# Kernel tuning notes

Hardware: AMD Instinct MI355X
Metric: run time of the kernel (lower is better)

The kernel has to match this reference:

```python
import jax, jax.numpy as jnp
import numpy as np

N, E, G, D, L = 100000, 1600000, 64, 128, 4
CLS_HID, NUM_CLASSES = 256, 10
BN_EPS = 1e-5


def setup_inputs() -> dict:
    key = jax.random.key(0)
    ks = jax.random.split(key, 16)
    s = 0.05
    cls_in = D + L * D  # sum(dims) = 640
    return {
        "node_deg": jax.random.randint(ks[0], (N,), 0, D),
        "edge_index": jax.random.randint(ks[1], (2, E), 0, N),
        "batch_vec": jnp.sort(jax.random.randint(ks[2], (N,), 0, G)),
        "eps": jnp.zeros((L,), jnp.float32),  # GINConv train_eps init 0
        "W1": jax.random.normal(ks[3], (L, D, D), jnp.float32) * s,
        "b1": jax.random.normal(ks[4], (L, D), jnp.float32) * s,
        "W2": jax.random.normal(ks[5], (L, D, D), jnp.float32) * s,
        "b2": jax.random.normal(ks[6], (L, D), jnp.float32) * s,
        "bn_g": jnp.ones((L, D), jnp.float32),
        "bn_b": jnp.zeros((L, D), jnp.float32),
        "Wc1": jax.random.normal(ks[7], (cls_in, CLS_HID), jnp.float32) * s,
        "bc1": jax.random.normal(ks[8], (CLS_HID,), jnp.float32) * s,
        "Wc2": jax.random.normal(ks[9], (CLS_HID, NUM_CLASSES), jnp.float32) * s,
        "bc2": jax.random.normal(ks[10], (NUM_CLASSES,), jnp.float32) * s,
    }


def reference(node_deg, edge_index, batch_vec, eps, W1, b1, W2, b2, bn_g, bn_b, Wc1, bc1, Wc2, bc2):
    n = node_deg.shape[0]
    src, dst = edge_index[0], edge_index[1]
    # OneHotEmbedding of node degree -> initial node features [N, D]
    x = jax.nn.one_hot(node_deg, D, dtype=jnp.float32)
    zs = [x]
    for l in range(eps.shape[0]):
        h_in = zs[-1]
        # GINConv: (1+eps)*x + scatter-add of neighbor features
        agg = jax.ops.segment_sum(h_in[src], dst, num_segments=n)
        h = (1.0 + eps[l]) * h_in + agg
        # mlp: lin -> lrelu -> lin
        h = jax.nn.leaky_relu(h @ W1[l] + b1[l])
        h = h @ W2[l] + b2[l]
        # BatchNorm1d over nodes (training-mode batch stats, biased var)
        mean = h.mean(axis=0)
        var = h.var(axis=0)
        h = (h - mean) * jax.lax.rsqrt(var + BN_EPS) * bn_g[l] + bn_b[l]
        zs.append(jax.nn.leaky_relu(h))
    z = jnp.concatenate(zs, axis=1)  # [N, 640]
    pooled = jax.ops.segment_sum(z, batch_vec, num_segments=G)  # global_add_pool
    pooled = jax.nn.leaky_relu(pooled)
    # classifier head: Linear -> LeakyReLU -> Linear (drop_out=0)
    h = jax.nn.leaky_relu(pooled @ Wc1 + bc1)
    return h @ Wc2 + bc2
```

## Files before the change

kernel.cpp:

```cpp
#include <hip/hip_runtime.h>
#include <hip/hip_bf16.h>


#define N_NODES   100000
#define N_EDGES   1600000
#define N_GRAPHS  64
#define DIM       128
#define N_LAYERS  4
#define CLS_IN    640
#define CLS_HID   256
#define N_CLASSES 10
#define LRELU_SLOPE 0.01f
#define BN_EPS_F    1e-5f

#define NBUCK    782
#define BUCK_CAP 4096

typedef __attribute__((ext_vector_type(8))) short bf16x8;
typedef __attribute__((ext_vector_type(4))) float f32x4;

__device__ __forceinline__ float lrelu(float x) { return x > 0.f ? x : LRELU_SLOPE * x; }

__device__ __forceinline__ uint pack2(float x, float y) {
    uint a = __float_as_uint(x), b = __float_as_uint(y);
    a = (a + 0x7FFFu + ((a >> 16) & 1u)) >> 16;
    b = (b + 0x7FFFu + ((b >> 16) & 1u)) >> 16;
    return a | (b << 16);
}
__device__ __forceinline__ float2 unpack2(uint v) {
    return make_float2(__uint_as_float(v << 16), __uint_as_float(v & 0xFFFF0000u));
}

__global__ void k_convert_w(const float* __restrict__ W1, const float* __restrict__ W2,
                            ushort* __restrict__ W1t, ushort* __restrict__ W2t) {
    int gid = blockIdx.x * blockDim.x + threadIdx.x;
    if (gid >= 8 * DIM * DIM) return;
    int mat = gid >> 14, idx = gid & 16383;
    int k = idx >> 7, n = idx & 127;
    const float* src = (mat < 4) ? (W1 + mat * DIM * DIM) : (W2 + (mat - 4) * DIM * DIM);
    ushort* dst = (mat < 4) ? (W1t + mat * DIM * DIM) : (W2t + (mat - 4) * DIM * DIM);
    uint a = __float_as_uint(src[k * DIM + n]);
    dst[n * DIM + k] = (ushort)((a + 0x7FFFu + ((a >> 16) & 1u)) >> 16);
}

__global__ void k_build_x(const int* __restrict__ deg, uint* __restrict__ x) {
    int gid = blockIdx.x * blockDim.x + threadIdx.x;
    if (gid >= N_NODES * 64) return;
    int i = gid >> 6, c = gid & 63;
    int d = deg[i];
    uint v = 0;
    if ((d >> 1) == c) v = 0x3F80u << (16 * (d & 1));
    x[gid] = v;
}

__global__ void k_deg_pool(const int* __restrict__ deg, const int* __restrict__ batch,
                           float* __restrict__ pooled) {
    int i = blockIdx.x * blockDim.x + threadIdx.x;
    if (i < N_NODES) atomicAdd(&pooled[batch[i] * CLS_IN + deg[i]], 1.0f);
}

__global__ void __launch_bounds__(1024) k_partition(const int* __restrict__ src,
                                                    const int* __restrict__ dst,
                                                    uint* __restrict__ cursor,
                                                    uint* __restrict__ ebuf) {
    __shared__ uint hist[NBUCK];
    __shared__ uint basev[NBUCK];
    int t = threadIdx.x;
    for (int b = t; b < NBUCK; b += 1024) hist[b] = 0;
    __syncthreads();
    int e0 = blockIdx.x * 16384;
    uint msrc[16], mdst[16], mrank[16];
#pragma unroll
    for (int i = 0; i < 16; ++i) {
        int e = e0 + i * 1024 + t;
        if (e < N_EDGES) {
            msrc[i] = (uint)src[e];
            mdst[i] = (uint)dst[e];
            mrank[i] = atomicAdd(&hist[mdst[i] >> 7], 1u);
        } else mdst[i] = 0xFFFFFFFFu;
    }
    __syncthreads();
    for (int b = t; b < NBUCK; b += 1024) {
        uint c = hist[b];
        basev[b] = c ? (uint)(b * BUCK_CAP) + atomicAdd(&cursor[b], c) : 0u;
    }
    __syncthreads();
#pragma unroll
    for (int i = 0; i < 16; ++i) {
        if (mdst[i] != 0xFFFFFFFFu) {
            uint b = mdst[i] >> 7;
            ebuf[basev[b] + mrank[i]] = ((mdst[i] & 127u) << 17) | msrc[i];
        }
    }
}

__global__ void __launch_bounds__(512) k_agg(const uint* __restrict__ h,
                                             const uint* __restrict__ ebuf,
                                             const uint* __restrict__ cursor,
                                             uint* __restrict__ out,
                                             const float* __restrict__ epsv, int layer) {
    __shared__ uint sortedL[BUCK_CAP];
    __shared__ uint hist[128];
    __shared__ uint startv[129];
    const int t = threadIdx.x, lane = t & 63, wave = t >> 6;
    const int b = blockIdx.x;
    int cnt = (int)cursor[b]; if (cnt > BUCK_CAP) cnt = BUCK_CAP;
    if (t < 128) hist[t] = 0;
    __syncthreads();
    uint ent[8], rank[8];
    const uint* ep = ebuf + b * BUCK_CAP;
#pragma unroll
    for (int k = 0; k < 8; ++k) {
        int i = t + k * 512;
        if (i < cnt) { ent[k] = ep[i]; rank[k] = atomicAdd(&hist[ent[k] >> 17], 1u); }
    }
    __syncthreads();
    if (t < 128) startv[t + 1] = hist[t];
    if (t == 0) startv[0] = 0;
    __syncthreads();
    for (int off = 1; off < 128; off <<= 1) {
        uint add = (t < 128 && t >= off) ? startv[t + 1 - off] : 0u;
        __syncthreads();
        if (t < 128 && t >= off) startv[t + 1] += add;
        __syncthreads();
    }
#pragma unroll
    for (int k = 0; k < 8; ++k) {
        int i = t + k * 512;
        if (i < cnt) sortedL[startv[ent[k] >> 17] + rank[k]] = ent[k];
    }
    __syncthreads();
    const float s = 1.0f + epsv[layer];
    const int node0 = b * 128;
    for (int ri = 0; ri < 16; ++ri) {
        int r = wave * 16 + ri;
        int g = node0 + r;
        if (g >= N_NODES) break;
        int beg = (int)startv[r], end = (int)startv[r + 1];
        float2 own = unpack2(h[g * 64 + lane]);
        float ax = s * own.x, ay = s * own.y;
        int j = beg;
        for (; j + 4 <= end; j += 4) {
            uint u0 = sortedL[j]     & 0x1FFFFu;
            uint u1 = sortedL[j + 1] & 0x1FFFFu;
            uint u2 = sortedL[j + 2] & 0x1FFFFu;
            uint u3 = sortedL[j + 3] & 0x1FFFFu;
            uint h0 = h[u0 * 64 + lane], h1 = h[u1 * 64 + lane];
            uint h2 = h[u2 * 64 + lane], h3 = h[u3 * 64 + lane];
            float2 f0 = unpack2(h0), f1 = unpack2(h1), f2 = unpack2(h2), f3 = unpack2(h3);
            ax += (f0.x + f1.x) + (f2.x + f3.x);
            ay += (f0.y + f1.y) + (f2.y + f3.y);
        }
        for (; j < end; ++j) {
            uint u = sortedL[j] & 0x1FFFFu;
            float2 f = unpack2(h[u * 64 + lane]);
            ax += f.x; ay += f.y;
        }
        out[g * 64 + lane] = pack2(ax, ay);
    }
}

#define GEMM_LDS_BYTES 69632
__global__ void __launch_bounds__(256) k_gemm(const ushort* __restrict__ A,
                                              const ushort* __restrict__ Wt,
                                              const float* __restrict__ bias,
                                              ushort* __restrict__ C,
                                              float* __restrict__ stats,
                                              int do_lrelu) {
    __shared__ char pool[GEMM_LDS_BYTES];
    ushort* As = (ushort*)pool;
    ushort* Ws = (ushort*)(pool + 34816);
    float*  Cs = (float*)pool;
    const int t = threadIdx.x;
    const int row0 = blockIdx.x * 128;
    {
        int r = t >> 1, hh = t & 1;
        uint4* l = (uint4*)(As + r * 136 + hh * 64);
        if (row0 + r < N_NODES) {
            const uint4* g = (const uint4*)(A + (size_t)(row0 + r) * DIM + hh * 64);
#pragma unroll
            for (int k = 0; k < 8; ++k) l[k] = g[k];
        } else {
            uint4 z = make_uint4(0, 0, 0, 0);
#pragma unroll
            for (int k = 0; k < 8; ++k) l[k] = z;
        }
        const uint4* gw = (const uint4*)(Wt + r * DIM + hh * 64);
        uint4* lw = (uint4*)(Ws + r * 136 + hh * 64);
#pragma unroll
        for (int k = 0; k < 8; ++k) lw[k] = gw[k];
    }
    __syncthreads();
    const int lane = t & 63, wave = t >> 6;
    const int q = lane >> 4, m = lane & 15;
    const int R = (wave >> 1) * 64, Cb = (wave & 1) * 64;
    f32x4 acc[4][4] = {};
#pragma unroll
    for (int ks = 0; ks < 4; ++ks) {
        bf16x8 a[4], b[4];
#pragma unroll
        for (int i = 0; i < 4; ++i)
            a[i] = *(const bf16x8*)(As + (R + i * 16 + m) * 136 + ks * 32 + q * 8);
#pragma unroll
        for (int j = 0; j < 4; ++j)
            b[j] = *(const bf16x8*)(Ws + (Cb + j * 16 + m) * 136 + ks * 32 + q * 8);
#pragma unroll
        for (int i = 0; i < 4; ++i)
#pragma unroll
            for (int j = 0; j < 4; ++j)
                acc[i][j] = __builtin_amdgcn_mfma_f32_16x16x32_bf16(a[i], b[j], acc[i][j], 0, 0, 0);
    }
    __syncthreads();
    float biasr[4];
#pragma unroll
    for (int j = 0; j < 4; ++j) biasr[j] = bias[Cb + j * 16 + m];
#pragma unroll
    for (int i = 0; i < 4; ++i)
#pragma unroll
        for (int j = 0; j < 4; ++j)
#pragma unroll
            for (int r = 0; r < 4; ++r)
                Cs[(R + i * 16 + q * 4 + r) * 132 + Cb + j * 16 + m] = acc[i][j][r] + biasr[j];
    __syncthreads();
    if (stats != nullptr && t < DIM) {
        int rows = N_NODES - row0; if (rows > 128) rows = 128;
        float s1 = 0.f, s2 = 0.f;
        for (int r = 0; r < rows; ++r) { float v = Cs[r * 132 + t]; s1 += v; s2 += v * v; }
        atomicAdd(&stats[t], s1);
        atomicAdd(&stats[DIM + t], s2);
    }
    {
        int r = t >> 1, hh = t & 1;
        if (row0 + r < N_NODES) {
            uint4* outp = (uint4*)(C + (size_t)(row0 + r) * DIM + hh * 64);
#pragma unroll
            for (int k = 0; k < 8; ++k) {
                float4 v0 = *(const float4*)(Cs + r * 132 + hh * 64 + k * 8);
                float4 v1 = *(const float4*)(Cs + r * 132 + hh * 64 + k * 8 + 4);
                if (do_lrelu) {
                    v0.x = lrelu(v0.x); v0.y = lrelu(v0.y); v0.z = lrelu(v0.z); v0.w = lrelu(v0.w);
                    v1.x = lrelu(v1.x); v1.y = lrelu(v1.y); v1.z = lrelu(v1.z); v1.w = lrelu(v1.w);
                }
                uint4 o;
                o.x = pack2(v0.x, v0.y); o.y = pack2(v0.z, v0.w);
                o.z = pack2(v1.x, v1.y); o.w = pack2(v1.z, v1.w);
                outp[k] = o;
            }
        }
    }
}

__global__ void k_bn_final(float* __restrict__ stats, const float* __restrict__ bn_g,
                           const float* __restrict__ bn_b, int layer) {
    int f = threadIdx.x;
    float mean = stats[f] * (1.0f / N_NODES);
    float var  = stats[DIM + f] * (1.0f / N_NODES) - mean * mean;
    float inv  = rsqrtf(var + BN_EPS_F);
    float sc = bn_g[layer * DIM + f] * inv;
    float sh = bn_b[layer * DIM + f] - mean * sc;
    stats[f] = sc;
    stats[DIM + f] = sh;
}

#define PROWS 128
__global__ void __launch_bounds__(256) k_bnpool(const uint* __restrict__ src,
                                                uint* __restrict__ dst,
                                                const float* __restrict__ stats,
                                                const int* __restrict__ batch,
                                                float* __restrict__ pooled, int colOff) {
    int c = threadIdx.x & 63;
    int chunk = threadIdx.x >> 6;
    int r0 = blockIdx.x * PROWS + chunk * (PROWS / 4);
    float sc0 = stats[2 * c], sc1 = stats[2 * c + 1];
    float sh0 = stats[DIM + 2 * c], sh1 = stats[DIM + 2 * c + 1];
    int curg = -1;
    float a0 = 0.f, a1 = 0.f;
    for (int i = 0; i < PROWS / 4; ++i) {
        int r = r0 + i;
        if (r >= N_NODES) break;
        float2 v = unpack2(src[r * 64 + c]);
        float x0 = lrelu(v.x * sc0 + sh0);
        float x1 = lrelu(v.y * sc1 + sh1);
        dst[r * 64 + c] = pack2(x0, x1);
        int g = batch[r];
        if (g != curg) {
            if (curg >= 0) {
                atomicAdd(&pooled[curg * CLS_IN + colOff + 2 * c], a0);
                atomicAdd(&pooled[curg * CLS_IN + colOff + 2 * c + 1], a1);
            }
            curg = g; a0 = 0.f; a1 = 0.f;
        }
        a0 += x0; a1 += x1;
    }
    if (curg >= 0) {
        atomicAdd(&pooled[curg * CLS_IN + colOff + 2 * c], a0);
        atomicAdd(&pooled[curg * CLS_IN + colOff + 2 * c + 1], a1);
    }
}

__global__ void __launch_bounds__(256) k_classifier(const float* __restrict__ pooled,
                                                    const float* __restrict__ Wc1,
                                                    const float* __restrict__ bc1,
                                                    const float* __restrict__ Wc2,
                                                    const float* __restrict__ bc2,
                                                    float* __restrict__ out) {
    __shared__ float p[CLS_IN];
    __shared__ float hh[CLS_HID];
    int g = blockIdx.x, t = threadIdx.x;
    for (int j = t; j < CLS_IN; j += 256) p[j] = lrelu(pooled[g * CLS_IN + j]);
    __syncthreads();
    float acc = bc1[t];
    for (int k = 0; k < CLS_IN; ++k) acc += p[k] * Wc1[k * CLS_HID + t];
    hh[t] = lrelu(acc);
    __syncthreads();
    if (t < N_CLASSES) {
        float a2 = bc2[t];
        for (int k = 0; k < CLS_HID; ++k) a2 += hh[k] * Wc2[k * N_CLASSES + t];
        out[g * N_CLASSES + t] = a2;
    }
}

extern "C" void kernel_launch(void* const* d_in, const int* in_sizes, int n_in,
                              void* d_out, int out_size, void* d_ws, size_t ws_size,
                              hipStream_t stream) {
    const int*   deg   = (const int*)d_in[0];
    const int*   edges = (const int*)d_in[1];
    const int*   srcv  = edges;
    const int*   dstv  = edges + N_EDGES;
    const int*   batch = (const int*)d_in[2];
    const float* epsv  = (const float*)d_in[3];
    const float* W1    = (const float*)d_in[4];
    const float* b1    = (const float*)d_in[5];
    const float* W2    = (const float*)d_in[6];
    const float* b2    = (const float*)d_in[7];
    const float* bn_g  = (const float*)d_in[8];
    const float* bn_b  = (const float*)d_in[9];
    const float* Wc1   = (const float*)d_in[10];
    const float* bc1   = (const float*)d_in[11];
    const float* Wc2   = (const float*)d_in[12];
    const float* bc2   = (const float*)d_in[13];

    char* ws = (char*)d_ws;
    const size_t BUFB = (size_t)N_NODES * DIM * 2;
    size_t off = 0;
    ushort* buf0   = (ushort*)(ws + off); off += BUFB;
    ushort* buf1   = (ushort*)(ws + off); off += BUFB;
    ushort* W1t    = (ushort*)(ws + off); off += 4 * DIM * DIM * 2;
    ushort* W2t    = (ushort*)(ws + off); off += 4 * DIM * DIM * 2;
    float*  pooled = (float*)(ws + off);  off += N_GRAPHS * CLS_IN * 4;
    float*  statsA = (float*)(ws + off);  off += 4 * 2 * DIM * 4;
    uint*   cursor = (uint*)(ws + off);   off += (NBUCK + 8) * 4;
    uint*   ebuf   = (uint*)(ws + off);   off += (size_t)NBUCK * BUCK_CAP * 4;

    hipMemsetAsync(pooled, 0, N_GRAPHS * CLS_IN * 4, stream);
    hipMemsetAsync(statsA, 0, 4 * 2 * DIM * 4, stream);
    hipMemsetAsync(cursor, 0, NBUCK * 4, stream);

    k_convert_w<<<(8 * DIM * DIM + 255) / 256, 256, 0, stream>>>(W1, W2, W1t, W2t);
    k_build_x<<<(N_NODES * 64 + 255) / 256, 256, 0, stream>>>(deg, (uint*)buf0);
    k_deg_pool<<<(N_NODES + 255) / 256, 256, 0, stream>>>(deg, batch, pooled);
    k_partition<<<(N_EDGES + 16383) / 16384, 1024, 0, stream>>>(srcv, dstv, cursor, ebuf);

    const int gemm_grid = (N_NODES + 127) / 128;
    for (int l = 0; l < N_LAYERS; ++l) {
        float* stats = statsA + l * 2 * DIM;
        k_agg<<<NBUCK, 512, 0, stream>>>((const uint*)buf0, ebuf, cursor,
                                         (uint*)buf1, epsv, l);
        k_gemm<<<gemm_grid, 256, 0, stream>>>(buf1, W1t + l * DIM * DIM, b1 + l * DIM,
                                              buf1, nullptr, 1);
        k_gemm<<<gemm_grid, 256, 0, stream>>>(buf1, W2t + l * DIM * DIM, b2 + l * DIM,
                                              buf1, stats, 0);
        k_bn_final<<<1, DIM, 0, stream>>>(stats, bn_g, bn_b, l);
        k_bnpool<<<(N_NODES + PROWS - 1) / PROWS, 256, 0, stream>>>(
            (const uint*)buf1, (uint*)buf0, stats, batch, pooled, DIM * (l + 1));
    }

    k_classifier<<<N_GRAPHS, 256, 0, stream>>>(pooled, Wc1, bc1, Wc2, bc2, (float*)d_out);
}
```

Baseline: 721.5 us.

## Build global CSR once, fuse two GEMMs into one MLP kernel, fold BN finalize

Per-bucket edge sorting is hoisted out of the layer loop: a one-time sort kernel writes a global CSR (indptr plus source indices), and the per-layer aggregation just reads it instead of re-sorting each bucket in LDS. The two per-layer GEMM launches are merged into a single MLP kernel that keeps the hidden activation in LDS, removing a global round trip and a launch. The BN finalize kernel is folded into the bnpool kernel, and the degree-pool kernel is folded into the one-hot build. The trade-off is extra workspace, an added setup pass, and more LDS and register pressure in the fused MLP kernel.

```diff
diff --git a/kernel.cpp b/kernel.cpp
--- a/kernel.cpp
+++ b/kernel.cpp
@@ -21,6 +21,10 @@
 
 __device__ __forceinline__ float lrelu(float x) { return x > 0.f ? x : LRELU_SLOPE * x; }
 
+__device__ __forceinline__ ushort bf16r(float x) {
+    uint a = __float_as_uint(x);
+    return (ushort)((a + 0x7FFFu + ((a >> 16) & 1u)) >> 16);
+}
 __device__ __forceinline__ uint pack2(float x, float y) {
     uint a = __float_as_uint(x), b = __float_as_uint(y);
     a = (a + 0x7FFFu + ((a >> 16) & 1u)) >> 16;
@@ -39,11 +43,11 @@
     int k = idx >> 7, n = idx & 127;
     const float* src = (mat < 4) ? (W1 + mat * DIM * DIM) : (W2 + (mat - 4) * DIM * DIM);
     ushort* dst = (mat < 4) ? (W1t + mat * DIM * DIM) : (W2t + (mat - 4) * DIM * DIM);
-    uint a = __float_as_uint(src[k * DIM + n]);
-    dst[n * DIM + k] = (ushort)((a + 0x7FFFu + ((a >> 16) & 1u)) >> 16);
-}
-
-__global__ void k_build_x(const int* __restrict__ deg, uint* __restrict__ x) {
+    dst[n * DIM + k] = bf16r(src[k * DIM + n]);
+}
+
+__global__ void k_build_x(const int* __restrict__ deg, const int* __restrict__ batch,
+                          uint* __restrict__ x, float* __restrict__ pooled) {
     int gid = blockIdx.x * blockDim.x + threadIdx.x;
     if (gid >= N_NODES * 64) return;
     int i = gid >> 6, c = gid & 63;
@@ -51,12 +55,7 @@
     uint v = 0;
     if ((d >> 1) == c) v = 0x3F80u << (16 * (d & 1));
     x[gid] = v;
-}
-
-__global__ void k_deg_pool(const int* __restrict__ deg, const int* __restrict__ batch,
-                           float* __restrict__ pooled) {
-    int i = blockIdx.x * blockDim.x + threadIdx.x;
-    if (i < N_NODES) atomicAdd(&pooled[batch[i] * CLS_IN + deg[i]], 1.0f);
+    if (c == 0) atomicAdd(&pooled[batch[i] * CLS_IN + d], 1.0f);
 }
 
 __global__ void __launch_bounds__(1024) k_partition(const int* __restrict__ src,
@@ -94,16 +93,32 @@
     }
 }
 
-__global__ void __launch_bounds__(512) k_agg(const uint* __restrict__ h,
-                                             const uint* __restrict__ ebuf,
-                                             const uint* __restrict__ cursor,
-                                             uint* __restrict__ out,
-                                             const float* __restrict__ epsv, int layer) {
+__global__ void __launch_bounds__(1024) k_bases(const uint* __restrict__ cursor,
+                                                uint* __restrict__ base,
+                                                int* __restrict__ indptr) {
+    __shared__ uint sh[1024];
+    int t = threadIdx.x;
+    uint v = (t < NBUCK) ? min(cursor[t], (uint)BUCK_CAP) : 0u;
+    sh[t] = v; __syncthreads();
+    for (int off = 1; off < 1024; off <<= 1) {
+        uint add = (t >= off) ? sh[t - off] : 0u;
+        __syncthreads();
+        sh[t] += add;
+        __syncthreads();
+    }
+    if (t < NBUCK) base[t] = sh[t] - v;
+    if (t == NBUCK - 1) indptr[N_NODES] = (int)sh[t];
+}
+
+__global__ void __launch_bounds__(512) k_sort(const uint* __restrict__ ebuf,
+                                              const uint* __restrict__ cursor,
+                                              const uint* __restrict__ base,
+                                              int* __restrict__ csr,
+                                              int* __restrict__ indptr) {
     __shared__ uint sortedL[BUCK_CAP];
     __shared__ uint hist[128];
     __shared__ uint startv[129];
-    const int t = threadIdx.x, lane = t & 63, wave = t >> 6;
-    const int b = blockIdx.x;
+    const int t = threadIdx.x, b = blockIdx.x;
     int cnt = (int)cursor[b]; if (cnt > BUCK_CAP) cnt = BUCK_CAP;
     if (t < 128) hist[t] = 0;
     __syncthreads();
@@ -130,29 +145,40 @@
         if (i < cnt) sortedL[startv[ent[k] >> 17] + rank[k]] = ent[k];
     }
     __syncthreads();
+    int gbase = (int)base[b];
+    for (int i = t; i < cnt; i += 512)
+        csr[gbase + i] = (int)(sortedL[i] & 0x1FFFFu);
+    if (t < 128) {
+        int node = b * 128 + t;
+        if (node < N_NODES) indptr[node] = gbase + (int)startv[t];
+    }
+}
+
+__global__ void __launch_bounds__(512) k_agg3(const uint* __restrict__ h,
+                                              const int* __restrict__ indptr,
+                                              const int* __restrict__ csr,
+                                              uint* __restrict__ out,
+                                              const float* __restrict__ epsv, int layer) {
+    const int t = threadIdx.x, lane = t & 63, wave = t >> 6;
     const float s = 1.0f + epsv[layer];
-    const int node0 = b * 128;
+    const int node0 = blockIdx.x * 128 + wave * 16;
     for (int ri = 0; ri < 16; ++ri) {
-        int r = wave * 16 + ri;
-        int g = node0 + r;
+        int g = node0 + ri;
         if (g >= N_NODES) break;
-        int beg = (int)startv[r], end = (int)startv[r + 1];
+        int beg = indptr[g], end = indptr[g + 1];
         float2 own = unpack2(h[g * 64 + lane]);
         float ax = s * own.x, ay = s * own.y;
         int j = beg;
         for (; j + 4 <= end; j += 4) {
-            uint u0 = sortedL[j]     & 0x1FFFFu;
-            uint u1 = sortedL[j + 1] & 0x1FFFFu;
-            uint u2 = sortedL[j + 2] & 0x1FFFFu;
-            uint u3 = sortedL[j + 3] & 0x1FFFFu;
-            uint h0 = h[u0 * 64 + lane], h1 = h[u1 * 64 + lane];
-            uint h2 = h[u2 * 64 + lane], h3 = h[u3 * 64 + lane];
-            float2 f0 = unpack2(h0), f1 = unpack2(h1), f2 = unpack2(h2), f3 = unpack2(h3);
+            int i0 = csr[j], i1 = csr[j + 1], i2 = csr[j + 2], i3 = csr[j + 3];
+            uint w0 = h[i0 * 64 + lane], w1 = h[i1 * 64 + lane];
+            uint w2 = h[i2 * 64 + lane], w3 = h[i3 * 64 + lane];
+            float2 f0 = unpack2(w0), f1 = unpack2(w1), f2 = unpack2(w2), f3 = unpack2(w3);
             ax += (f0.x + f1.x) + (f2.x + f3.x);
             ay += (f0.y + f1.y) + (f2.y + f3.y);
         }
         for (; j < end; ++j) {
-            uint u = sortedL[j] & 0x1FFFFu;
+            int u = csr[j];
             float2 f = unpack2(h[u * 64 + lane]);
             ax += f.x; ay += f.y;
         }
@@ -160,14 +186,15 @@
     }
 }
 
-#define GEMM_LDS_BYTES 69632
-__global__ void __launch_bounds__(256) k_gemm(const ushort* __restrict__ A,
-                                              const ushort* __restrict__ Wt,
-                                              const float* __restrict__ bias,
-                                              ushort* __restrict__ C,
-                                              float* __restrict__ stats,
-                                              int do_lrelu) {
-    __shared__ char pool[GEMM_LDS_BYTES];
+#define MLP_LDS_BYTES 69632
+__global__ void __launch_bounds__(256) k_mlp(const ushort* __restrict__ A,
+                                             const ushort* __restrict__ W1t,
+                                             const float* __restrict__ b1,
+                                             const ushort* __restrict__ W2t,
+                                             const float* __restrict__ b2,
+                                             ushort* __restrict__ C,
+                                             float* __restrict__ stats) {
+    __shared__ char pool[MLP_LDS_BYTES];
     ushort* As = (ushort*)pool;
     ushort* Ws = (ushort*)(pool + 34816);
     float*  Cs = (float*)pool;
@@ -185,7 +212,7 @@
 #pragma unroll
             for (int k = 0; k < 8; ++k) l[k] = z;
         }
-        const uint4* gw = (const uint4*)(Wt + r * DIM + hh * 64);
+        const uint4* gw = (const uint4*)(W1t + r * DIM + hh * 64);
         uint4* lw = (uint4*)(Ws + r * 136 + hh * 64);
 #pragma unroll
         for (int k = 0; k < 8; ++k) lw[k] = gw[k];
@@ -194,7 +221,45 @@
     const int lane = t & 63, wave = t >> 6;
     const int q = lane >> 4, m = lane & 15;
     const int R = (wave >> 1) * 64, Cb = (wave & 1) * 64;
-    f32x4 acc[4][4] = {};
+    {
+        f32x4 acc[4][4] = {};
+#pragma unroll
+        for (int ks = 0; ks < 4; ++ks) {
+            bf16x8 a[4], b[4];
+#pragma unroll
+            for (int i = 0; i < 4; ++i)
+                a[i] = *(const bf16x8*)(As + (R + i * 16 + m) * 136 + ks * 32 + q * 8);
+#pragma unroll
+            for (int j = 0; j < 4; ++j)
+                b[j] = *(const bf16x8*)(Ws + (Cb + j * 16 + m) * 136 + ks * 32 + q * 8);
+#pragma unroll
+            for (int i = 0; i < 4; ++i)
+#pragma unroll
+                for (int j = 0; j < 4; ++j)
+                    acc[i][j] = __builtin_amdgcn_mfma_f32_16x16x32_bf16(a[i], b[j], acc[i][j], 0, 0, 0);
+        }
+        __syncthreads();
+        float bias1[4];
+#pragma unroll
+        for (int j = 0; j < 4; ++j) bias1[j] = b1[Cb + j * 16 + m];
+#pragma unroll
+        for (int i = 0; i < 4; ++i)
+#pragma unroll
+            for (int j = 0; j < 4; ++j)
+#pragma unroll
+                for (int r = 0; r < 4; ++r)
+                    As[(R + i * 16 + q * 4 + r) * 136 + Cb + j * 16 + m] =
+                        bf16r(lrelu(acc[i][j][r] + bias1[j]));
+        {
+            int r = t >> 1, hh = t & 1;
+            const uint4* gw = (const uint4*)(W2t + r * DIM + hh * 64);
+            uint4* lw = (uint4*)(Ws + r * 136 + hh * 64);
+#pragma unroll
+            for (int k = 0; k < 8; ++k) lw[k] = gw[k];
+        }
+    }
+    __syncthreads();
+    f32x4 acc2[4][4] = {};
 #pragma unroll
     for (int ks = 0; ks < 4; ++ks) {
         bf16x8 a[4], b[4];
@@ -208,21 +273,21 @@
         for (int i = 0; i < 4; ++i)
 #pragma unroll
             for (int j = 0; j < 4; ++j)
-                acc[i][j] = __builtin_amdgcn_mfma_f32_16x16x32_bf16(a[i], b[j], acc[i][j], 0, 0, 0);
-    }
-    __syncthreads();
-    float biasr[4];
-#pragma unroll
-    for (int j = 0; j < 4; ++j) biasr[j] = bias[Cb + j * 16 + m];
+                acc2[i][j] = __builtin_amdgcn_mfma_f32_16x16x32_bf16(a[i], b[j], acc2[i][j], 0, 0, 0);
+    }
+    __syncthreads();
+    float bias2[4];
+#pragma unroll
+    for (int j = 0; j < 4; ++j) bias2[j] = b2[Cb + j * 16 + m];
 #pragma unroll
     for (int i = 0; i < 4; ++i)
 #pragma unroll
         for (int j = 0; j < 4; ++j)
 #pragma unroll
             for (int r = 0; r < 4; ++r)
-                Cs[(R + i * 16 + q * 4 + r) * 132 + Cb + j * 16 + m] = acc[i][j][r] + biasr[j];
-    __syncthreads();
-    if (stats != nullptr && t < DIM) {
+                Cs[(R + i * 16 + q * 4 + r) * 132 + Cb + j * 16 + m] = acc2[i][j][r] + bias2[j];
+    __syncthreads();
+    if (t < DIM) {
         int rows = N_NODES - row0; if (rows > 128) rows = 128;
         float s1 = 0.f, s2 = 0.f;
         for (int r = 0; r < rows; ++r) { float v = Cs[r * 132 + t]; s1 += v; s2 += v * v; }
@@ -237,10 +302,6 @@
             for (int k = 0; k < 8; ++k) {
                 float4 v0 = *(const float4*)(Cs + r * 132 + hh * 64 + k * 8);
                 float4 v1 = *(const float4*)(Cs + r * 132 + hh * 64 + k * 8 + 4);
-                if (do_lrelu) {
-                    v0.x = lrelu(v0.x); v0.y = lrelu(v0.y); v0.z = lrelu(v0.z); v0.w = lrelu(v0.w);
-                    v1.x = lrelu(v1.x); v1.y = lrelu(v1.y); v1.z = lrelu(v1.z); v1.w = lrelu(v1.w);
-                }
                 uint4 o;
                 o.x = pack2(v0.x, v0.y); o.y = pack2(v0.z, v0.w);
                 o.z = pack2(v1.x, v1.y); o.w = pack2(v1.z, v1.w);
@@ -250,29 +311,29 @@
     }
 }
 
-__global__ void k_bn_final(float* __restrict__ stats, const float* __restrict__ bn_g,
-                           const float* __restrict__ bn_b, int layer) {
-    int f = threadIdx.x;
-    float mean = stats[f] * (1.0f / N_NODES);
-    float var  = stats[DIM + f] * (1.0f / N_NODES) - mean * mean;
-    float inv  = rsqrtf(var + BN_EPS_F);
-    float sc = bn_g[layer * DIM + f] * inv;
-    float sh = bn_b[layer * DIM + f] - mean * sc;
-    stats[f] = sc;
-    stats[DIM + f] = sh;
-}
-
 #define PROWS 128
 __global__ void __launch_bounds__(256) k_bnpool(const uint* __restrict__ src,
                                                 uint* __restrict__ dst,
                                                 const float* __restrict__ stats,
+                                                const float* __restrict__ bn_g,
+                                                const float* __restrict__ bn_b, int layer,
                                                 const int* __restrict__ batch,
                                                 float* __restrict__ pooled, int colOff) {
     int c = threadIdx.x & 63;
     int chunk = threadIdx.x >> 6;
     int r0 = blockIdx.x * PROWS + chunk * (PROWS / 4);
-    float sc0 = stats[2 * c], sc1 = stats[2 * c + 1];
-    float sh0 = stats[DIM + 2 * c], sh1 = stats[DIM + 2 * c + 1];
+    float sc0, sh0, sc1, sh1;
+    {
+        int f0 = 2 * c, f1 = 2 * c + 1;
+        float m0 = stats[f0] * (1.0f / N_NODES);
+        float m1 = stats[f1] * (1.0f / N_NODES);
+        float v0 = stats[DIM + f0] * (1.0f / N_NODES) - m0 * m0;
+        float v1 = stats[DIM + f1] * (1.0f / N_NODES) - m1 * m1;
+        sc0 = bn_g[layer * DIM + f0] * rsqrtf(v0 + BN_EPS_F);
+        sc1 = bn_g[layer * DIM + f1] * rsqrtf(v1 + BN_EPS_F);
+        sh0 = bn_b[layer * DIM + f0] - m0 * sc0;
+        sh1 = bn_b[layer * DIM + f1] - m1 * sc1;
+    }
     int curg = -1;
     float a0 = 0.f, a1 = 0.f;
     for (int i = 0; i < PROWS / 4; ++i) {
@@ -350,6 +411,9 @@
     float*  pooled = (float*)(ws + off);  off += N_GRAPHS * CLS_IN * 4;
     float*  statsA = (float*)(ws + off);  off += 4 * 2 * DIM * 4;
     uint*   cursor = (uint*)(ws + off);   off += (NBUCK + 8) * 4;
+    uint*   base   = (uint*)(ws + off);   off += (NBUCK + 8) * 4;
+    int*    indptr = (int*)(ws + off);    off += (N_NODES + 8) * 4;
+    int*    csr    = (int*)(ws + off);    off += (size_t)N_EDGES * 4;
     uint*   ebuf   = (uint*)(ws + off);   off += (size_t)NBUCK * BUCK_CAP * 4;
 
     hipMemsetAsync(pooled, 0, N_GRAPHS * CLS_IN * 4, stream);
@@ -357,22 +421,22 @@
     hipMemsetAsync(cursor, 0, NBUCK * 4, stream);
 
     k_convert_w<<<(8 * DIM * DIM + 255) / 256, 256, 0, stream>>>(W1, W2, W1t, W2t);
-    k_build_x<<<(N_NODES * 64 + 255) / 256, 256, 0, stream>>>(deg, (uint*)buf0);
-    k_deg_pool<<<(N_NODES + 255) / 256, 256, 0, stream>>>(deg, batch, pooled);
+    k_build_x<<<(N_NODES * 64 + 255) / 256, 256, 0, stream>>>(deg, batch, (uint*)buf0, pooled);
     k_partition<<<(N_EDGES + 16383) / 16384, 1024, 0, stream>>>(srcv, dstv, cursor, ebuf);
+    k_bases<<<1, 1024, 0, stream>>>(cursor, base, indptr);
+    k_sort<<<NBUCK, 512, 0, stream>>>(ebuf, cursor, base, csr, indptr);
 
     const int gemm_grid = (N_NODES + 127) / 128;
     for (int l = 0; l < N_LAYERS; ++l) {
         float* stats = statsA + l * 2 * DIM;
-        k_agg<<<NBUCK, 512, 0, stream>>>((const uint*)buf0, ebuf, cursor,
-                                         (uint*)buf1, epsv, l);
-        k_gemm<<<gemm_grid, 256, 0, stream>>>(buf1, W1t + l * DIM * DIM, b1 + l * DIM,
-                                              buf1, nullptr, 1);
-        k_gemm<<<gemm_grid, 256, 0, stream>>>(buf1, W2t + l * DIM * DIM, b2 + l * DIM,
-                                              buf1, stats, 0);
-        k_bn_final<<<1, DIM, 0, stream>>>(stats, bn_g, bn_b, l);
+        k_agg3<<<NBUCK, 512, 0, stream>>>((const uint*)buf0, indptr, csr,
+                                          (uint*)buf1, epsv, l);
+        k_mlp<<<gemm_grid, 256, 0, stream>>>(buf1, W1t + l * DIM * DIM, b1 + l * DIM,
+                                             W2t + l * DIM * DIM, b2 + l * DIM,
+                                             buf1, stats);
         k_bnpool<<<(N_NODES + PROWS - 1) / PROWS, 256, 0, stream>>>(
-            (const uint*)buf1, (uint*)buf0, stats, batch, pooled, DIM * (l + 1));
+            (const uint*)buf1, (uint*)buf0, stats, bn_g, bn_b, l, batch,
+            pooled, DIM * (l + 1));
     }
 
     k_classifier<<<N_GRAPHS, 256, 0, stream>>>(pooled, Wc1, bc1, Wc2, bc2, (float*)d_out);
```

Result: slower. 751.1 us (+4.1%).
